# Kernel optimization log

Hardware: AMD Instinct MI355X
Metric: run time of the kernel (lower is better)

The kernel has to match this reference:

```python
import jax, jax.numpy as jnp
import numpy as np

B, S, D, H = 4, 2048, 1024, 16
HD = D // H

def rotate_half(x):
    x1, x2 = jnp.split(x, 2, axis=-1)
    return jnp.concatenate((-x2, x1), axis=-1)

def apply_rope(x, cos, sin):
    # x: [B,H,S,hd]; cos/sin: [S,hd] -> broadcast over B,H
    return x * cos[None, None] + rotate_half(x) * sin[None, None]

def setup_inputs() -> dict:
    key = jax.random.key(0)
    ks = jax.random.split(key, 8)
    x = jax.random.normal(ks[0], (B, S, D), dtype=jnp.float32)
    mask = jnp.triu(jnp.ones((S, S), dtype=bool), k=1)  # True = masked (causal)
    pos = jnp.arange(S, dtype=jnp.float32)[:, None]
    inv = 1.0 / (10000.0 ** (jnp.arange(0, HD, 2, dtype=jnp.float32) / HD))
    ang = pos * inv[None, :]  # [S, hd/2]
    ang = jnp.concatenate([ang, ang], axis=-1)  # [S, hd]
    rope_cos = jnp.cos(ang)
    rope_sin = jnp.sin(ang)
    scale = 1.0 / np.sqrt(D)
    Wq = jax.random.normal(ks[1], (D, D), dtype=jnp.float32) * scale
    Wk = jax.random.normal(ks[2], (D, D), dtype=jnp.float32) * scale
    Wv = jax.random.normal(ks[3], (D, D), dtype=jnp.float32) * scale
    Wo = jax.random.normal(ks[4], (D, D), dtype=jnp.float32) * scale
    z = jnp.zeros((D,), dtype=jnp.float32)
    return {"x": x, "mask": mask, "rope_cos": rope_cos, "rope_sin": rope_sin,
            "Wq": Wq, "bq": z, "Wk": Wk, "bk": z, "Wv": Wv, "bv": z, "Wo": Wo, "bo": z}

def reference(x, mask, rope_cos, rope_sin, Wq, bq, Wk, bk, Wv, bv, Wo, bo):
    b, s, d = x.shape
    def proj(W, bias):
        y = x @ W.T + bias  # torch Linear: x W^T + b
        return y.reshape(b, s, H, HD).transpose(0, 2, 1, 3)  # [B,H,S,hd]
    Q = apply_rope(proj(Wq, bq), rope_cos, rope_sin)
    K = apply_rope(proj(Wk, bk), rope_cos, rope_sin)
    V = proj(Wv, bv)
    scores = jnp.einsum('bhqd,bhkd->bhqk', Q, K) / jnp.sqrt(jnp.float32(HD))
    scores = jnp.where(mask[None, None], -jnp.inf, scores)
    attn = jax.nn.softmax(scores, axis=-1)
    ctx = jnp.einsum('bhqk,bhkd->bhqd', attn, V)
    ctx = ctx.transpose(0, 2, 1, 3).reshape(b, s, d)
    return ctx @ Wo.T + bo
```

## Files before the change

kernel.cpp:

```cpp
#include <hip/hip_runtime.h>
#include <hip/hip_bf16.h>

#define S_LEN 2048
#define D_MODEL 1024
#define NH 16
#define HDIM 64
#define B_SZ 4

typedef __attribute__((ext_vector_type(8))) short bf16x8;
typedef __attribute__((ext_vector_type(4))) float f32x4;

__device__ inline void gld16(const __hip_bfloat16* g, __hip_bfloat16* l) {
    __builtin_amdgcn_global_load_lds(
        (const __attribute__((address_space(1))) unsigned int*)g,
        (__attribute__((address_space(3))) unsigned int*)l, 16, 0, 0);
}

__device__ inline unsigned int pkbf(float a, float b) {
    float2 f; f.x = a; f.y = b;
    __hip_bfloat162 h = __float22bfloat162_rn(f);
    union { __hip_bfloat162 h; unsigned int u; } cv; cv.h = h; return cv.u;
}

__global__ __launch_bounds__(256) void f2bf4_kernel(const float4* __restrict__ in,
                                                    __hip_bfloat162* __restrict__ out,
                                                    int n4) {
    int i = blockIdx.x * 256 + threadIdx.x;
    if (i < n4) {
        float4 v = in[i];
        __hip_bfloat162 a, b;
        a.x = __float2bfloat16(v.x); a.y = __float2bfloat16(v.y);
        b.x = __float2bfloat16(v.z); b.y = __float2bfloat16(v.w);
        out[2 * i]     = a;
        out[2 * i + 1] = b;
    }
}

__global__ __launch_bounds__(256) void f2bfw_kernel(
    const float4* __restrict__ w0, const float4* __restrict__ w1,
    const float4* __restrict__ w2, const float4* __restrict__ w3,
    __hip_bfloat162* __restrict__ o0, __hip_bfloat162* __restrict__ o1,
    __hip_bfloat162* __restrict__ o2, __hip_bfloat162* __restrict__ o3) {
    const int z = blockIdx.y;
    const float4* in = (z == 0) ? w0 : (z == 1) ? w1 : (z == 2) ? w2 : w3;
    __hip_bfloat162* out = (z == 0) ? o0 : (z == 1) ? o1 : (z == 2) ? o2 : o3;
    int i = blockIdx.x * 256 + threadIdx.x;
    float4 v = in[i];
    __hip_bfloat162 a, b;
    a.x = __float2bfloat16(v.x); a.y = __float2bfloat16(v.y);
    b.x = __float2bfloat16(v.z); b.y = __float2bfloat16(v.w);
    out[2 * i]     = a;
    out[2 * i + 1] = b;
}

__device__ inline void gemm_mainloop(const __hip_bfloat16* __restrict__ X,
                                     const __hip_bfloat16* __restrict__ W,
                                     __hip_bfloat16* As, __hip_bfloat16* Bs,
                                     int m0, int n0, f32x4 acc[4][4]) {
    const int tid = threadIdx.x;
    const int wv = tid >> 6, lane = tid & 63, l15 = lane & 15, quad = lane >> 4;
    const int rw = (wv >> 1) * 64, cw = (wv & 1) * 64;
    for (int k0 = 0; k0 < D_MODEL; k0 += 32) {
        __syncthreads();
#pragma unroll
        for (int i = 0; i < 2; i++) {
            int l = tid + 256 * i;
            int row = l >> 2, c8 = (l & 3) * 8;
            gld16(&X[(size_t)(m0 + row) * D_MODEL + k0 + c8], &As[row * 32 + c8]);
            gld16(&W[(size_t)(n0 + row) * D_MODEL + k0 + c8], &Bs[row * 32 + c8]);
        }
        __syncthreads();
        bf16x8 af[4], bfr[4];
#pragma unroll
        for (int t = 0; t < 4; t++)
            af[t] = *(const bf16x8*)&As[(rw + t * 16 + l15) * 32 + quad * 8];
#pragma unroll
        for (int t = 0; t < 4; t++)
            bfr[t] = *(const bf16x8*)&Bs[(cw + t * 16 + l15) * 32 + quad * 8];
#pragma unroll
        for (int mt = 0; mt < 4; mt++)
#pragma unroll
            for (int nt = 0; nt < 4; nt++)
                acc[mt][nt] = __builtin_amdgcn_mfma_f32_16x16x32_bf16(
                    af[mt], bfr[nt], acc[mt][nt], 0, 0, 0);
    }
}

__global__ __launch_bounds__(256) void qkv_kernel(
    const __hip_bfloat16* __restrict__ X,
    const __hip_bfloat16* __restrict__ W0, const __hip_bfloat16* __restrict__ W1,
    const __hip_bfloat16* __restrict__ W2,
    const float* __restrict__ b0, const float* __restrict__ b1,
    const float* __restrict__ b2,
    const float* __restrict__ rc, const float* __restrict__ rs,
    __hip_bfloat16* __restrict__ Qo, __hip_bfloat16* __restrict__ Ko,
    __hip_bfloat16* __restrict__ Vo) {
    __shared__ __hip_bfloat16 As[128 * 32];
    __shared__ __hip_bfloat16 Bs[128 * 32];
    const int z = blockIdx.z;
    const __hip_bfloat16* W = (z == 0) ? W0 : ((z == 1) ? W1 : W2);
    const float* bias = (z == 0) ? b0 : ((z == 1) ? b1 : b2);
    f32x4 acc[4][4];
#pragma unroll
    for (int i = 0; i < 4; i++)
#pragma unroll
        for (int j = 0; j < 4; j++) acc[i][j] = (f32x4){0.f, 0.f, 0.f, 0.f};
    const int m0 = blockIdx.x * 128, n0 = blockIdx.y * 128;
    gemm_mainloop(X, W, As, Bs, m0, n0, acc);

    const int tid = threadIdx.x;
    const int wv = tid >> 6, lane = tid & 63, l15 = lane & 15, quad = lane >> 4;
    const int rw = (wv >> 1) * 64, cw = (wv & 1) * 64;

    if (z == 2) {
#pragma unroll
        for (int mt = 0; mt < 4; mt++)
#pragma unroll
            for (int r = 0; r < 4; r++) {
                int m = m0 + rw + mt * 16 + quad * 4 + r;
                int s = m & (S_LEN - 1), b = m >> 11;
#pragma unroll
                for (int nt = 0; nt < 4; nt++) {
                    int n = n0 + cw + nt * 16 + l15;
                    int h = n >> 6, hd = n & 63;
                    float v = acc[mt][nt][r] + bias[n];
                    Vo[(((size_t)(b * NH + h)) * S_LEN + s) * HDIM + hd] =
                        __float2bfloat16(v);
                }
            }
    } else {
        __hip_bfloat16* dst = (z == 0) ? Qo : Ko;
        const float qs = (z == 0) ? 0.18033688011112042f : 1.0f;
#pragma unroll
        for (int mt = 0; mt < 4; mt++)
#pragma unroll
            for (int r = 0; r < 4; r++) {
                int m = m0 + rw + mt * 16 + quad * 4 + r;
                int s = m & (S_LEN - 1), b = m >> 11;
#pragma unroll
                for (int nt = 0; nt < 2; nt++) {
                    int n1 = n0 + cw + nt * 16 + l15;
                    int h = n1 >> 6, hd1 = n1 & 63;
                    float y1 = acc[mt][nt][r] + bias[n1];
                    float y2 = acc[mt][nt + 2][r] + bias[n1 + 32];
                    float c1 = rc[s * HDIM + hd1], s1 = rs[s * HDIM + hd1];
                    float c2 = rc[s * HDIM + hd1 + 32], s2 = rs[s * HDIM + hd1 + 32];
                    size_t base = (((size_t)(b * NH + h)) * S_LEN + s) * HDIM;
                    dst[base + hd1]      = __float2bfloat16((y1 * c1 - y2 * s1) * qs);
                    dst[base + hd1 + 32] = __float2bfloat16((y2 * c2 + y1 * s2) * qs);
                }
            }
    }
}

#define SWZ(r, c) (((r) << 6) + ((c) ^ (((r) & 7) << 3)))
__global__ __launch_bounds__(256) void attn_kernel(
    const __hip_bfloat16* __restrict__ Q, const __hip_bfloat16* __restrict__ K,
    const __hip_bfloat16* __restrict__ V, __hip_bfloat16* __restrict__ CTX) {
    __shared__ __hip_bfloat16 Kl[64 * 64];
    __shared__ __hip_bfloat16 Vt[64 * 64];
    __shared__ __hip_bfloat16 Pl[2][4][16 * 64];
    const int tid = threadIdx.x;
    const int wv = tid >> 6, lane = tid & 63, l15 = lane & 15, quad = lane >> 4;
    const int bh = blockIdx.x;
    const int pr = blockIdx.y;
    const int tA = pr, tC = 31 - pr;
    const int nkb = tC + 1;
    const size_t off = (size_t)bh * S_LEN * HDIM;
    const __hip_bfloat16* Qp = Q + off;
    const __hip_bfloat16* Kp = K + off;
    const __hip_bfloat16* Vp = V + off;
    __hip_bfloat16* PC = &Pl[0][wv][0];
    __hip_bfloat16* PA = &Pl[1][wv][0];

    bf16x8 qfA[2], qfC[2];
#pragma unroll
    for (int c = 0; c < 2; c++) {
        qfA[c] = *(const bf16x8*)&Qp[(size_t)(tA * 64 + wv * 16 + l15) * HDIM + c * 32 + quad * 8];
        qfC[c] = *(const bf16x8*)&Qp[(size_t)(tC * 64 + wv * 16 + l15) * HDIM + c * 32 + quad * 8];
    }

    float lA = 0.f, lC = 0.f;
    f32x4 accA[4], accC[4];
#pragma unroll
    for (int nt = 0; nt < 4; nt++) {
        accA[nt] = (f32x4){0.f, 0.f, 0.f, 0.f};
        accC[nt] = (f32x4){0.f, 0.f, 0.f, 0.f};
    }

    float4 kreg[2];
    unsigned short vreg[16];
    auto load_tile = [&](int kb) {
        const int k0 = kb * 64;
#pragma unroll
        for (int i = 0; i < 2; i++) {
            int l = tid + 256 * i;
            kreg[i] = *(const float4*)&Kp[(size_t)(k0 + (l >> 3)) * HDIM + (l & 7) * 8];
        }
#pragma unroll
        for (int j = 0; j < 16; j++)
            vreg[j] = *(const unsigned short*)&Vp[(size_t)(k0 + wv * 16 + j) * HDIM + lane];
    };
    auto store_tile = [&]() {
#pragma unroll
        for (int i = 0; i < 2; i++) {
            int l = tid + 256 * i;
            *(float4*)&Kl[SWZ(l >> 3, (l & 7) * 8)] = kreg[i];
        }
        union { bf16x8 v; unsigned short u[8]; } p0, p1;
#pragma unroll
        for (int j = 0; j < 8; j++) { p0.u[j] = vreg[j]; p1.u[j] = vreg[8 + j]; }
        *(bf16x8*)&Vt[SWZ(lane, wv * 16)]     = p0.v;
        *(bf16x8*)&Vt[SWZ(lane, wv * 16 + 8)] = p1.v;
    };

    const int qrel = wv * 16 + l15;

    load_tile(0);
    for (int kb = 0; kb < nkb; kb++) {
        __syncthreads();
        store_tile();
        __syncthreads();
        if (kb + 1 < nkb) load_tile(kb + 1);

        const bool aAct = (kb <= tA);
        unsigned int pkC[8], pkA[8];

        f32x4 saC[4], saA[4];
#pragma unroll
        for (int st = 0; st < 4; st++) {
            saC[st] = (f32x4){0.f, 0.f, 0.f, 0.f};
            saA[st] = (f32x4){0.f, 0.f, 0.f, 0.f};
        }
        if (aAct) {
#pragma unroll
            for (int c = 0; c < 2; c++)
#pragma unroll
                for (int st = 0; st < 4; st++) {
                    bf16x8 kf = *(const bf16x8*)&Kl[SWZ(st * 16 + l15, c * 32 + quad * 8)];
                    saC[st] = __builtin_amdgcn_mfma_f32_16x16x32_bf16(kf, qfC[c], saC[st], 0, 0, 0);
                    saA[st] = __builtin_amdgcn_mfma_f32_16x16x32_bf16(kf, qfA[c], saA[st], 0, 0, 0);
                }
        } else {
#pragma unroll
            for (int c = 0; c < 2; c++)
#pragma unroll
                for (int st = 0; st < 4; st++) {
                    bf16x8 kf = *(const bf16x8*)&Kl[SWZ(st * 16 + l15, c * 32 + quad * 8)];
                    saC[st] = __builtin_amdgcn_mfma_f32_16x16x32_bf16(kf, qfC[c], saC[st], 0, 0, 0);
                }
        }

        {
            float ls = 0.f;
            if (kb == tC) {
#pragma unroll
                for (int st = 0; st < 4; st++) {
                    float p[4];
#pragma unroll
                    for (int r = 0; r < 4; r++) {
                        bool msk = (st * 16 + quad * 4 + r > qrel);
                        p[r] = msk ? 0.f : __builtin_exp2f(saC[st][r]);
                        ls += p[r];
                    }
                    pkC[st * 2 + 0] = pkbf(p[0], p[1]);
                    pkC[st * 2 + 1] = pkbf(p[2], p[3]);
                }
            } else {
#pragma unroll
                for (int st = 0; st < 4; st++) {
                    float p[4];
#pragma unroll
                    for (int r = 0; r < 4; r++) {
                        p[r] = __builtin_exp2f(saC[st][r]);
                        ls += p[r];
                    }
                    pkC[st * 2 + 0] = pkbf(p[0], p[1]);
                    pkC[st * 2 + 1] = pkbf(p[2], p[3]);
                }
            }
            ls += __shfl_xor(ls, 16);
            ls += __shfl_xor(ls, 32);
            lC += ls;
#pragma unroll
            for (int st = 0; st < 4; st++) {
                uint2 w; w.x = pkC[st * 2]; w.y = pkC[st * 2 + 1];
                *(uint2*)&PC[SWZ(l15, st * 16 + quad * 4)] = w;
            }
        }
        if (aAct) {
            float ls = 0.f;
            if (kb == tA) {
#pragma unroll
                for (int st = 0; st < 4; st++) {
                    float p[4];
#pragma unroll
                    for (int r = 0; r < 4; r++) {
                        bool msk = (st * 16 + quad * 4 + r > qrel);
                        p[r] = msk ? 0.f : __builtin_exp2f(saA[st][r]);
                        ls += p[r];
                    }
                    pkA[st * 2 + 0] = pkbf(p[0], p[1]);
                    pkA[st * 2 + 1] = pkbf(p[2], p[3]);
                }
            } else {
#pragma unroll
                for (int st = 0; st < 4; st++) {
                    float p[4];
#pragma unroll
                    for (int r = 0; r < 4; r++) {
                        p[r] = __builtin_exp2f(saA[st][r]);
                        ls += p[r];
                    }
                    pkA[st * 2 + 0] = pkbf(p[0], p[1]);
                    pkA[st * 2 + 1] = pkbf(p[2], p[3]);
                }
            }
            ls += __shfl_xor(ls, 16);
            ls += __shfl_xor(ls, 32);
            lA += ls;
#pragma unroll
            for (int st = 0; st < 4; st++) {
                uint2 w; w.x = pkA[st * 2]; w.y = pkA[st * 2 + 1];
                *(uint2*)&PA[SWZ(l15, st * 16 + quad * 4)] = w;
            }
        }

#pragma unroll
        for (int c = 0; c < 2; c++) {
            bf16x8 vf[4];
#pragma unroll
            for (int nt = 0; nt < 4; nt++)
                vf[nt] = *(const bf16x8*)&Vt[SWZ(nt * 16 + l15, c * 32 + quad * 8)];
            {
                bf16x8 pf = *(const bf16x8*)&PC[SWZ(l15, c * 32 + quad * 8)];
#pragma unroll
                for (int nt = 0; nt < 4; nt++)
                    accC[nt] = __builtin_amdgcn_mfma_f32_16x16x32_bf16(vf[nt], pf, accC[nt], 0, 0, 0);
            }
            if (aAct) {
                bf16x8 pf = *(const bf16x8*)&PA[SWZ(l15, c * 32 + quad * 8)];
#pragma unroll
                for (int nt = 0; nt < 4; nt++)
                    accA[nt] = __builtin_amdgcn_mfma_f32_16x16x32_bf16(vf[nt], pf, accA[nt], 0, 0, 0);
            }
        }
    }

    const int b = bh >> 4, h = bh & 15;
    {
        const int q = tA * 64 + wv * 16 + l15;
        const float inv = 1.0f / lA;
#pragma unroll
        for (int nt = 0; nt < 4; nt++) {
            uint2 st2;
            st2.x = pkbf(accA[nt][0] * inv, accA[nt][1] * inv);
            st2.y = pkbf(accA[nt][2] * inv, accA[nt][3] * inv);
            *(uint2*)&CTX[((size_t)(b * S_LEN + q)) * D_MODEL + h * HDIM + nt * 16 + quad * 4] = st2;
        }
    }
    {
        const int q = tC * 64 + wv * 16 + l15;
        const float inv = 1.0f / lC;
#pragma unroll
        for (int nt = 0; nt < 4; nt++) {
            uint2 st2;
            st2.x = pkbf(accC[nt][0] * inv, accC[nt][1] * inv);
            st2.y = pkbf(accC[nt][2] * inv, accC[nt][3] * inv);
            *(uint2*)&CTX[((size_t)(b * S_LEN + q)) * D_MODEL + h * HDIM + nt * 16 + quad * 4] = st2;
        }
    }
}

__global__ __launch_bounds__(256) void outproj_kernel(
    const __hip_bfloat16* __restrict__ X, const __hip_bfloat16* __restrict__ W,
    const float* __restrict__ bias, float* __restrict__ OUT) {
    __shared__ __hip_bfloat16 As[128 * 32];
    __shared__ __hip_bfloat16 Bs[128 * 32];
    f32x4 acc[4][4];
#pragma unroll
    for (int i = 0; i < 4; i++)
#pragma unroll
        for (int j = 0; j < 4; j++) acc[i][j] = (f32x4){0.f, 0.f, 0.f, 0.f};
    const int m0 = blockIdx.x * 128, n0 = blockIdx.y * 128;
    gemm_mainloop(X, W, As, Bs, m0, n0, acc);
    const int tid = threadIdx.x;
    const int wv = tid >> 6, lane = tid & 63, l15 = lane & 15, quad = lane >> 4;
    const int rw = (wv >> 1) * 64, cw = (wv & 1) * 64;
#pragma unroll
    for (int mt = 0; mt < 4; mt++)
#pragma unroll
        for (int r = 0; r < 4; r++) {
            int m = m0 + rw + mt * 16 + quad * 4 + r;
#pragma unroll
            for (int nt = 0; nt < 4; nt++) {
                int n = n0 + cw + nt * 16 + l15;
                OUT[(size_t)m * D_MODEL + n] = acc[mt][nt][r] + bias[n];
            }
        }
}

extern "C" void kernel_launch(void* const* d_in, const int* in_sizes, int n_in,
                              void* d_out, int out_size, void* d_ws, size_t ws_size,
                              hipStream_t stream) {
    const float* x  = (const float*)d_in[0];
    const float* rc = (const float*)d_in[2];
    const float* rs = (const float*)d_in[3];
    const float* Wq = (const float*)d_in[4];
    const float* bq = (const float*)d_in[5];
    const float* Wk = (const float*)d_in[6];
    const float* bk = (const float*)d_in[7];
    const float* Wv = (const float*)d_in[8];
    const float* bv = (const float*)d_in[9];
    const float* Wo = (const float*)d_in[10];
    const float* bo = (const float*)d_in[11];

    char* ws = (char*)d_ws;
    __hip_bfloat16* xbf = (__hip_bfloat16*)(ws);
    __hip_bfloat16* wqb = (__hip_bfloat16*)(ws + (16u << 20));
    __hip_bfloat16* wkb = (__hip_bfloat16*)(ws + (18u << 20));
    __hip_bfloat16* wvb = (__hip_bfloat16*)(ws + (20u << 20));
    __hip_bfloat16* wob = (__hip_bfloat16*)(ws + (22u << 20));
    __hip_bfloat16* Qb  = (__hip_bfloat16*)(ws + (24u << 20));
    __hip_bfloat16* Kb  = (__hip_bfloat16*)(ws + (40u << 20));
    __hip_bfloat16* Vb  = (__hip_bfloat16*)(ws + (56u << 20));
    __hip_bfloat16* Cb  = (__hip_bfloat16*)(ws + (72u << 20));
    float* out = (float*)d_out;

    f2bf4_kernel<<<8192, 256, 0, stream>>>((const float4*)x, (__hip_bfloat162*)xbf, 2097152);
    f2bfw_kernel<<<dim3(1024, 4), 256, 0, stream>>>(
        (const float4*)Wq, (const float4*)Wk, (const float4*)Wv, (const float4*)Wo,
        (__hip_bfloat162*)wqb, (__hip_bfloat162*)wkb, (__hip_bfloat162*)wvb,
        (__hip_bfloat162*)wob);

    qkv_kernel<<<dim3(64, 8, 3), 256, 0, stream>>>(xbf, wqb, wkb, wvb, bq, bk, bv,
                                                   rc, rs, Qb, Kb, Vb);
    attn_kernel<<<dim3(64, 16), 256, 0, stream>>>(Qb, Kb, Vb, Cb);
    outproj_kernel<<<dim3(64, 8), 256, 0, stream>>>(Cb, wob, bo, out);
}
```

Measured before the change: 337.5 us.

## Store V transposed from QKV and double-buffer attention K/V via async LDS loads

The QKV epilogue for V now stages the tile in shared memory and writes V transposed as [B,H,hd,S] with 16-byte coalesced stores, replacing scattered 2-byte stores. The attention kernel drops its register staging and in-kernel V transpose. It loads K and pre-transposed V tiles straight into double-buffered, pre-swizzled LDS with global_load_lds, so the next tile's fetch overlaps compute and one barrier per iteration is saved. s_setprio hints raise wave priority around the MFMA sections. This doubles LDS use in attention and relies on the async load being complete by the single end-of-loop barrier.

```diff
diff --git a/kernel.cpp b/kernel.cpp
--- a/kernel.cpp
+++ b/kernel.cpp
@@ -86,6 +86,7 @@
     }
 }
 
+#define PT 136
 __global__ __launch_bounds__(256) void qkv_kernel(
     const __hip_bfloat16* __restrict__ X,
     const __hip_bfloat16* __restrict__ W0, const __hip_bfloat16* __restrict__ W1,
@@ -95,8 +96,9 @@
     const float* __restrict__ rc, const float* __restrict__ rs,
     __hip_bfloat16* __restrict__ Qo, __hip_bfloat16* __restrict__ Ko,
     __hip_bfloat16* __restrict__ Vo) {
-    __shared__ __hip_bfloat16 As[128 * 32];
-    __shared__ __hip_bfloat16 Bs[128 * 32];
+    __shared__ __hip_bfloat16 pool[64 * PT];
+    __hip_bfloat16* As = pool;
+    __hip_bfloat16* Bs = pool + 4096;
     const int z = blockIdx.z;
     const __hip_bfloat16* W = (z == 0) ? W0 : ((z == 1) ? W1 : W2);
     const float* bias = (z == 0) ? b0 : ((z == 1) ? b1 : b2);
@@ -113,21 +115,34 @@
     const int rw = (wv >> 1) * 64, cw = (wv & 1) * 64;
 
     if (z == 2) {
-#pragma unroll
-        for (int mt = 0; mt < 4; mt++)
-#pragma unroll
-            for (int r = 0; r < 4; r++) {
-                int m = m0 + rw + mt * 16 + quad * 4 + r;
-                int s = m & (S_LEN - 1), b = m >> 11;
-#pragma unroll
-                for (int nt = 0; nt < 4; nt++) {
-                    int n = n0 + cw + nt * 16 + l15;
-                    int h = n >> 6, hd = n & 63;
-                    float v = acc[mt][nt][r] + bias[n];
-                    Vo[(((size_t)(b * NH + h)) * S_LEN + s) * HDIM + hd] =
-                        __float2bfloat16(v);
-                }
-            }
+        __hip_bfloat16* T = pool;
+        const int b = m0 >> 11, s0l = m0 & (S_LEN - 1);
+#pragma unroll
+        for (int hn = 0; hn < 2; hn++) {
+            __syncthreads();
+            if ((wv & 1) == hn) {
+#pragma unroll
+                for (int mt = 0; mt < 4; mt++)
+#pragma unroll
+                    for (int nt = 0; nt < 4; nt++)
+#pragma unroll
+                        for (int r = 0; r < 4; r++) {
+                            int dl = nt * 16 + l15;
+                            int ml = rw + mt * 16 + quad * 4 + r;
+                            T[dl * PT + ml] =
+                                __float2bfloat16(acc[mt][nt][r] + bias[n0 + hn * 64 + dl]);
+                        }
+            }
+            __syncthreads();
+            const int d = tid >> 2, sc = tid & 3;
+            const int h = (n0 >> 6) + hn;
+            size_t gb = ((size_t)((b * NH + h) * HDIM + d)) * S_LEN + s0l + sc * 32;
+#pragma unroll
+            for (int j = 0; j < 4; j++) {
+                bf16x8 v = *(const bf16x8*)&T[d * PT + sc * 32 + j * 8];
+                *(bf16x8*)&Vo[gb + j * 8] = v;
+            }
+        }
     } else {
         __hip_bfloat16* dst = (z == 0) ? Qo : Ko;
         const float qs = (z == 0) ? 0.18033688011112042f : 1.0f;
@@ -156,9 +171,9 @@
 #define SWZ(r, c) (((r) << 6) + ((c) ^ (((r) & 7) << 3)))
 __global__ __launch_bounds__(256) void attn_kernel(
     const __hip_bfloat16* __restrict__ Q, const __hip_bfloat16* __restrict__ K,
-    const __hip_bfloat16* __restrict__ V, __hip_bfloat16* __restrict__ CTX) {
-    __shared__ __hip_bfloat16 Kl[64 * 64];
-    __shared__ __hip_bfloat16 Vt[64 * 64];
+    const __hip_bfloat16* __restrict__ VT, __hip_bfloat16* __restrict__ CTX) {
+    __shared__ __hip_bfloat16 Kl[2][64 * 64];
+    __shared__ __hip_bfloat16 Vl[2][64 * 64];
     __shared__ __hip_bfloat16 Pl[2][4][16 * 64];
     const int tid = threadIdx.x;
     const int wv = tid >> 6, lane = tid & 63, l15 = lane & 15, quad = lane >> 4;
@@ -169,9 +184,27 @@
     const size_t off = (size_t)bh * S_LEN * HDIM;
     const __hip_bfloat16* Qp = Q + off;
     const __hip_bfloat16* Kp = K + off;
-    const __hip_bfloat16* Vp = V + off;
+    const __hip_bfloat16* Vp = VT + off;
     __hip_bfloat16* PC = &Pl[0][wv][0];
     __hip_bfloat16* PA = &Pl[1][wv][0];
+
+    const int e0 = wv * 512 + lane * 8;
+    const int r0 = e0 >> 6, c80 = e0 & 63;
+    const int sw0 = c80 ^ ((r0 & 7) << 3);
+    const int r1 = r0 + 32;
+    const int sw1 = c80 ^ ((r1 & 7) << 3);
+    const __hip_bfloat16* ks0 = Kp + r0 * 64 + sw0;
+    const __hip_bfloat16* ks1 = Kp + r1 * 64 + sw1;
+    const __hip_bfloat16* vs0 = Vp + (size_t)r0 * S_LEN + sw0;
+    const __hip_bfloat16* vs1 = Vp + (size_t)r1 * S_LEN + sw1;
+
+    auto stage = [&](int kb, int bsel) {
+        const int ko = kb * 64;
+        gld16(ks0 + (size_t)ko * 64, &Kl[bsel][e0]);
+        gld16(ks1 + (size_t)ko * 64, &Kl[bsel][e0 + 2048]);
+        gld16(vs0 + ko, &Vl[bsel][e0]);
+        gld16(vs1 + ko, &Vl[bsel][e0 + 2048]);
+    };
 
     bf16x8 qfA[2], qfC[2];
 #pragma unroll
@@ -188,40 +221,15 @@
         accC[nt] = (f32x4){0.f, 0.f, 0.f, 0.f};
     }
 
-    float4 kreg[2];
-    unsigned short vreg[16];
-    auto load_tile = [&](int kb) {
-        const int k0 = kb * 64;
-#pragma unroll
-        for (int i = 0; i < 2; i++) {
-            int l = tid + 256 * i;
-            kreg[i] = *(const float4*)&Kp[(size_t)(k0 + (l >> 3)) * HDIM + (l & 7) * 8];
-        }
-#pragma unroll
-        for (int j = 0; j < 16; j++)
-            vreg[j] = *(const unsigned short*)&Vp[(size_t)(k0 + wv * 16 + j) * HDIM + lane];
-    };
-    auto store_tile = [&]() {
-#pragma unroll
-        for (int i = 0; i < 2; i++) {
-            int l = tid + 256 * i;
-            *(float4*)&Kl[SWZ(l >> 3, (l & 7) * 8)] = kreg[i];
-        }
-        union { bf16x8 v; unsigned short u[8]; } p0, p1;
-#pragma unroll
-        for (int j = 0; j < 8; j++) { p0.u[j] = vreg[j]; p1.u[j] = vreg[8 + j]; }
-        *(bf16x8*)&Vt[SWZ(lane, wv * 16)]     = p0.v;
-        *(bf16x8*)&Vt[SWZ(lane, wv * 16 + 8)] = p1.v;
-    };
-
     const int qrel = wv * 16 + l15;
 
-    load_tile(0);
+    stage(0, 0);
+    __syncthreads();
     for (int kb = 0; kb < nkb; kb++) {
-        __syncthreads();
-        store_tile();
-        __syncthreads();
-        if (kb + 1 < nkb) load_tile(kb + 1);
+        const int buf = kb & 1;
+        if (kb + 1 < nkb) stage(kb + 1, buf ^ 1);
+        const __hip_bfloat16* Kb_ = &Kl[buf][0];
+        const __hip_bfloat16* Vb_ = &Vl[buf][0];
 
         const bool aAct = (kb <= tA);
         unsigned int pkC[8], pkA[8];
@@ -232,12 +240,13 @@
             saC[st] = (f32x4){0.f, 0.f, 0.f, 0.f};
             saA[st] = (f32x4){0.f, 0.f, 0.f, 0.f};
         }
+        __builtin_amdgcn_s_setprio(1);
         if (aAct) {
 #pragma unroll
             for (int c = 0; c < 2; c++)
 #pragma unroll
                 for (int st = 0; st < 4; st++) {
-                    bf16x8 kf = *(const bf16x8*)&Kl[SWZ(st * 16 + l15, c * 32 + quad * 8)];
+                    bf16x8 kf = *(const bf16x8*)&Kb_[SWZ(st * 16 + l15, c * 32 + quad * 8)];
                     saC[st] = __builtin_amdgcn_mfma_f32_16x16x32_bf16(kf, qfC[c], saC[st], 0, 0, 0);
                     saA[st] = __builtin_amdgcn_mfma_f32_16x16x32_bf16(kf, qfA[c], saA[st], 0, 0, 0);
                 }
@@ -246,10 +255,11 @@
             for (int c = 0; c < 2; c++)
 #pragma unroll
                 for (int st = 0; st < 4; st++) {
-                    bf16x8 kf = *(const bf16x8*)&Kl[SWZ(st * 16 + l15, c * 32 + quad * 8)];
+                    bf16x8 kf = *(const bf16x8*)&Kb_[SWZ(st * 16 + l15, c * 32 + quad * 8)];
                     saC[st] = __builtin_amdgcn_mfma_f32_16x16x32_bf16(kf, qfC[c], saC[st], 0, 0, 0);
                 }
         }
+        __builtin_amdgcn_s_setprio(0);
 
         {
             float ls = 0.f;
@@ -326,12 +336,13 @@
             }
         }
 
+        __builtin_amdgcn_s_setprio(1);
 #pragma unroll
         for (int c = 0; c < 2; c++) {
             bf16x8 vf[4];
 #pragma unroll
             for (int nt = 0; nt < 4; nt++)
-                vf[nt] = *(const bf16x8*)&Vt[SWZ(nt * 16 + l15, c * 32 + quad * 8)];
+                vf[nt] = *(const bf16x8*)&Vb_[SWZ(nt * 16 + l15, c * 32 + quad * 8)];
             {
                 bf16x8 pf = *(const bf16x8*)&PC[SWZ(l15, c * 32 + quad * 8)];
 #pragma unroll
@@ -345,6 +356,9 @@
                     accA[nt] = __builtin_amdgcn_mfma_f32_16x16x32_bf16(vf[nt], pf, accA[nt], 0, 0, 0);
             }
         }
+        __builtin_amdgcn_s_setprio(0);
+
+        __syncthreads();
     }
 
     const int b = bh >> 4, h = bh & 15;
```

Result: faster. 313.0 us (-7.3%).
